# Performance work log

Hardware: AMD Instinct MI355X
Metric: run time of the kernel (lower is better)

## Reference

```python
import jax, jax.numpy as jnp
import numpy as np

KERNEL = 9
EPS = 1e-5


def build_time_adj(t, kernel=KERNEL):
    # Faithful port of time_edge_index + utils.add_self_loops (all weights 1).
    # At[target, source] = 1 ; PyG edge list rows were [source=i, target=neighbor].
    p = (kernel - 1) // 2
    edges = []
    for i in range(t):
        if i < p:
            num_zeros_before = p - i
            elems = kernel - 1 - num_zeros_before
            before = i
            after = elems - before
            for j in range(before, 0, -1):
                edges.append((i, i - j))
            for j in range(after, 0, -1):
                edges.append((i, i + j))
        elif t - i <= p:
            num_zeros_after = p - (t - i) + 1
            elems = kernel - 1 - num_zeros_after
            before = kernel - 1 - p
            after = elems - before
            for j in range(before, 0, -1):
                edges.append((i, i - j))
            for j in range(after, 0, -1):
                edges.append((i, i + j))
        else:
            for j in range(1, p + 1):
                edges.append((i, i - j))
                edges.append((i, i + j))
    At = np.zeros((t, t), dtype=np.float32)
    for s, tg in edges:
        At[tg, s] = 1.0
    At[np.arange(t), np.arange(t)] = 1.0  # add_self_loops
    return At


def setup_inputs() -> dict:
    key = jax.random.key(0)
    ks = jax.random.split(key, 8)
    B, T, V, C = 64, 300, 25, 64
    x = jax.random.normal(ks[0], (B, T, V, C), dtype=jnp.float32)
    A = jax.random.uniform(ks[1], (3, V, V), dtype=jnp.float32)
    edge_importance = jnp.ones((3, V, V), dtype=jnp.float32)
    scale = 0.125  # ~xavier for 64x64
    W1 = jax.random.normal(ks[2], (C, C), dtype=jnp.float32) * scale
    W2 = jax.random.normal(ks[3], (C, C), dtype=jnp.float32) * scale
    W3 = jax.random.normal(ks[4], (C, C), dtype=jnp.float32) * scale
    Wt = jax.random.normal(ks[5], (C, C), dtype=jnp.float32) * scale
    b1 = jnp.zeros((C,), jnp.float32)
    b2 = jnp.zeros((C,), jnp.float32)
    b3 = jnp.zeros((C,), jnp.float32)
    bt = jnp.zeros((C,), jnp.float32)
    gamma = jnp.ones((C,), jnp.float32)
    beta = jnp.zeros((C,), jnp.float32)
    return {"x": x, "A": A, "edge_importance": edge_importance,
            "W1": W1, "b1": b1, "W2": W2, "b2": b2, "W3": W3, "b3": b3,
            "Wt": Wt, "bt": bt, "gamma": gamma, "beta": beta}


def reference(x, A, edge_importance, W1, b1, W2, b2, W3, b3, Wt, bt, gamma, beta):
    B, T, V, C = x.shape
    I = jnp.eye(V, dtype=x.dtype)
    Ae = A * edge_importance  # [3,V,V]

    # ---- Net_nodes: 3 spatial GCNConv branches summed (gcn_norm, self-loops) ----
    out = jnp.zeros((B, T, V, W1.shape[1]), dtype=x.dtype)
    for Ai, W, b in ((Ae[0], W1, b1), (Ae[1], W2, b2), (Ae[2], W3, b3)):
        Ad = Ai * (1.0 - I) + I                      # fill_diag(adj, 1.0)
        d = Ad.sum(axis=1)
        dinv = jnp.where(d > 0, d ** -0.5, 0.0)
        An = dinv[:, None] * Ad * dinv[None, :]      # D^-1/2 (A+I) D^-1/2
        out = out + jnp.einsum('vu,btuc->btvc', An, x @ W) + b

    def bn(h):  # BatchNorm2d over (B,T,V) per channel, training-mode stats
        m = h.mean(axis=(0, 1, 2))
        v = h.var(axis=(0, 1, 2))
        return (h - m) * jax.lax.rsqrt(v + EPS) * gamma + beta

    h = jax.nn.relu(bn(out))

    # ---- temporal GCNConv (normalize=False, unit edge weights, self loops) ----
    At = jnp.asarray(build_time_adj(T))              # [T,T] banded 0/1
    h = jnp.einsum('ts,bsvc->btvc', At, h @ Wt) + bt

    h = bn(h)  # same bn_2d module reused; dropout is identity in eval
    # residual=False, stride=1 -> x_res = 0, no sampling
    return jax.nn.relu(h)
```

## Files before the change

### kernel.cpp

```cpp
#include <hip/hip_runtime.h>

typedef unsigned short u16;
typedef unsigned int   u32;
typedef _Float16       f16;
typedef _Float16 f16x8 __attribute__((ext_vector_type(8)));
typedef float    f32x4 __attribute__((ext_vector_type(4)));

#define B_  64
#define T_  300
#define V_  25
#define C_  64
#define ROWS (B_*T_)
#define ROWE (V_*C_)
#define NSTAT 480000.0f
#define EPS_ 1e-5f
#define TTILE 30
#define K2GRID 4800

__device__ __forceinline__ float b2f(u16 u) {
    union { u32 i; float f; } v; v.i = ((u32)u) << 16; return v.f;
}
__device__ __forceinline__ u16 f2b(float f) {
    union { float f; u32 i; } v; v.f = f;
    u32 x = v.i;
    u32 r = x + 0x7fffu + ((x >> 16) & 1u);
    return (u16)(r >> 16);
}
__device__ __forceinline__ u32 pk2h(float a, float b) {
    union { f16 h[2]; u32 u; } p;
    p.h[0] = (f16)a; p.h[1] = (f16)b;
    return p.u;
}
__device__ __forceinline__ u16 h2u(float v) {
    union { f16 h; u16 u; } p; p.h = (f16)v; return p.u;
}
__device__ __forceinline__ float u2h(u16 u) {
    union { u16 u; f16 h; } p; p.u = u; return (float)p.h;
}

template<bool F32>
__device__ __forceinline__ float ldv(const void* p, size_t i) {
    if (F32) return ((const float*)p)[i];
    return b2f(((const u16*)p)[i]);
}

template<bool F32> struct Geo { static const int STR = F32 ? 3200 : 1600; };

__global__ void k0_detect(const void* W1raw, int* flag)
{
    __shared__ float red[256];
    const u16* p = (const u16*)W1raw;
    float mx = 0.0f;
    for (int i = threadIdx.x; i < 4096; i += 256) {
        float v = fabsf(b2f(p[i]));
        if (v == v) mx = fmaxf(mx, v);
    }
    red[threadIdx.x] = mx;
    __syncthreads();
    for (int s = 128; s > 0; s >>= 1) {
        if (threadIdx.x < s) red[threadIdx.x] = fmaxf(red[threadIdx.x], red[threadIdx.x + s]);
        __syncthreads();
    }
    if (threadIdx.x == 0) flag[0] = (red[0] > 1e10f) ? 1 : 0;
}

template<bool F32>
__global__ void k1_prep(const int* __restrict__ flag,
                        const void* A, const void* E,
                        const void* W1, const void* W2, const void* W3,
                        const void* Wt,
                        const void* b1, const void* b2, const void* b3,
                        u16* __restrict__ anf, u16* __restrict__ wcatT,
                        u16* __restrict__ wtT, float* __restrict__ bsum)
{
    if (flag[0] != (F32 ? 1 : 0)) return;
    __shared__ float dinvL[75];
    const int tid = threadIdx.x;
    if (tid < 75) {
        int i = tid / 25, v = tid % 25;
        float d = 1.0f;
        for (int u = 0; u < 25; ++u)
            if (u != v) d += ldv<F32>(A, (i*25+v)*25+u) * ldv<F32>(E, (i*25+v)*25+u);
        dinvL[tid] = (d > 0.0f) ? rsqrtf(d) : 0.0f;
    }
    __syncthreads();
    for (int idx = tid; idx < 3072; idx += 256) {
        int fr = idx >> 9, lane = (idx >> 3) & 63, j = idx & 7;
        int i = fr >> 1, nt = fr & 1;
        int v = nt*16 + (lane & 15);
        int u = ((lane >> 4) << 3) + j;
        float val = 0.0f;
        if (v < 25 && u < 25) {
            float ad = (u == v) ? 1.0f
                     : ldv<F32>(A, (i*25+v)*25+u) * ldv<F32>(E, (i*25+v)*25+u);
            val = dinvL[i*25+v] * ad * dinvL[i*25+u];
        }
        anf[idx] = h2u(val);
    }
    for (int idx = tid; idx < 13824; idx += 256) {
        int i = idx / 4608;
        int rem = idx - i*4608;
        int c = rem / 72, k = rem - (rem/72)*72;
        float val = 0.0f;
        if (k < 64) {
            const void* W = (i == 0) ? W1 : ((i == 1) ? W2 : W3);
            val = ldv<F32>(W, k*64 + c);
        }
        wcatT[idx] = h2u(val);
    }
    for (int idx = tid; idx < 4608; idx += 256) {
        int c = idx / 72, k = idx - (idx/72)*72;
        float val = (k < 64) ? ldv<F32>(Wt, k*64 + c) : 0.0f;
        wtT[idx] = h2u(val);
    }
    if (tid < 64) bsum[tid] = ldv<F32>(b1, tid) + ldv<F32>(b2, tid) + ldv<F32>(b3, tid);
}

template<bool F32>
__global__ __launch_bounds__(256, 3) void k2_mfma(
    const int* __restrict__ flag, const void* x,
    const u16* __restrict__ wcatT, const u16* __restrict__ anf,
    const float* __restrict__ bsum,
    u16* __restrict__ out1, float* __restrict__ p1)
{
    if (flag[0] != (F32 ? 1 : 0)) return;
    const int STR = Geo<F32>::STR;

    __shared__ f16 xf[112*72];
    __shared__ u16 xw[256*40];

    const int tid  = threadIdx.x;
    const int lane = tid & 63, w = tid >> 6;
    const int r0   = blockIdx.x * 4;

    for (int q4 = tid; q4 < 1600; q4 += 256) {
        int r = (q4 * 10486) >> 22;
        int rem = q4 - 400*r;
        float v0, v1, v2, v3;
        if (F32) {
            float4 t4 = ((const float4*)x)[(size_t)(r0+r)*400 + rem];
            v0 = t4.x; v1 = t4.y; v2 = t4.z; v3 = t4.w;
        } else {
            ushort4 t4 = ((const ushort4*)x)[(size_t)(r0+r)*400 + rem];
            v0 = b2f(t4.x); v1 = b2f(t4.y); v2 = b2f(t4.z); v3 = b2f(t4.w);
        }
        int u = rem >> 4, k0 = (rem & 15) << 2;
        int m = r*28 + u;
        *(uint2*)&xf[m*72 + k0] = make_uint2(pk2h(v0, v1), pk2h(v2, v3));
    }
    for (int idx = tid; idx < 432; idx += 256) {
        int j  = (idx * 57) >> 11;
        int off = idx - 36*j;
        int rr = (j*11) >> 5, p = j - 3*rr;
        ((u32*)xf)[(rr*28 + 25 + p)*36 + off] = 0u;
    }
    *(uint2*)&xw[tid*40 + 28] = make_uint2(0u, 0u);

    f16x8 anfr[3][2];
    #pragma unroll
    for (int i = 0; i < 3; ++i)
        #pragma unroll
        for (int nt = 0; nt < 2; ++nt)
            anfr[i][nt] = *(const f16x8*)&anf[((i*2 + nt)*64 + lane)*8];

    const int c0 = w*16 + ((lane >> 4) << 2);
    float bs[4];
    #pragma unroll
    for (int t = 0; t < 4; ++t) bs[t] = bsum[c0 + t];

    f32x4 acc[4][2];
    #pragma unroll
    for (int j = 0; j < 4; ++j) {
        acc[j][0] = f32x4{0.f, 0.f, 0.f, 0.f};
        acc[j][1] = f32x4{0.f, 0.f, 0.f, 0.f};
    }

    __syncthreads();

    #pragma unroll
    for (int i = 0; i < 3; ++i) {
        f16x8 wfr[4][2];
        #pragma unroll
        for (int nt = 0; nt < 4; ++nt)
            #pragma unroll
            for (int ks = 0; ks < 2; ++ks)
                wfr[nt][ks] = *(const f16x8*)&wcatT[
                    (i*64 + nt*16 + (lane & 15))*72 + ks*32 + ((lane >> 4) << 3)];

        for (int mt = w; mt < 7; mt += 4) {
            const int arow = (mt*16 + (lane & 15))*72 + ((lane >> 4) << 3);
            f16x8 a0 = *(const f16x8*)&xf[arow];
            f16x8 a1 = *(const f16x8*)&xf[arow + 32];
            const int m0 = mt*16 + ((lane >> 4) << 2);
            const int r  = (m0 * 293) >> 13;
            const int u0 = m0 - 28*r;
            #pragma unroll
            for (int nt = 0; nt < 4; ++nt) {
                f32x4 d = f32x4{0.f, 0.f, 0.f, 0.f};
                d = __builtin_amdgcn_mfma_f32_16x16x32_f16(a0, wfr[nt][0], d, 0, 0, 0);
                d = __builtin_amdgcn_mfma_f32_16x16x32_f16(a1, wfr[nt][1], d, 0, 0, 0);
                const int cc = nt*16 + (lane & 15);
                *(uint2*)&xw[(r*64 + cc)*40 + u0] =
                    make_uint2(pk2h(d[0], d[1]), pk2h(d[2], d[3]));
            }
        }
        __syncthreads();

        #pragma unroll
        for (int j = 0; j < 4; ++j) {
            const int mt2 = w + 4*j;
            f16x8 a = *(const f16x8*)&xw[(mt2*16 + (lane & 15))*40 + ((lane >> 4) << 3)];
            acc[j][0] = __builtin_amdgcn_mfma_f32_16x16x32_f16(a, anfr[i][0], acc[j][0], 0, 0, 0);
            acc[j][1] = __builtin_amdgcn_mfma_f32_16x16x32_f16(a, anfr[i][1], acc[j][1], 0, 0, 0);
        }
        __syncthreads();
    }

    float ssum[4] = {0.f, 0.f, 0.f, 0.f}, ssq[4] = {0.f, 0.f, 0.f, 0.f};
    const int vb = lane & 15;
    #pragma unroll
    for (int j = 0; j < 4; ++j) {
        #pragma unroll
        for (int nt = 0; nt < 2; ++nt) {
            const int v = nt*16 + vb;
            if (v < 25) {
                float o0 = acc[j][nt][0] + bs[0];
                float o1 = acc[j][nt][1] + bs[1];
                float o2 = acc[j][nt][2] + bs[2];
                float o3 = acc[j][nt][3] + bs[3];
                ssum[0] += o0; ssq[0] += o0*o0;
                ssum[1] += o1; ssq[1] += o1*o1;
                ssum[2] += o2; ssq[2] += o2*o2;
                ssum[3] += o3; ssq[3] += o3*o3;
                ushort4 pk;
                pk.x = f2b(o0); pk.y = f2b(o1); pk.z = f2b(o2); pk.w = f2b(o3);
                *(ushort4*)&out1[(size_t)(r0 + j)*STR + v*64 + c0] = pk;
            }
        }
    }
    #pragma unroll
    for (int t = 0; t < 4; ++t) {
        #pragma unroll
        for (int off = 1; off < 16; off <<= 1) {
            ssum[t] += __shfl_xor(ssum[t], off);
            ssq[t]  += __shfl_xor(ssq[t],  off);
        }
    }
    if ((lane & 15) == 0) {
        #pragma unroll
        for (int t = 0; t < 4; ++t) {
            p1[(size_t)blockIdx.x*128 + c0 + t]      = ssum[t];
            p1[(size_t)blockIdx.x*128 + 64 + c0 + t] = ssq[t];
        }
    }
}

template<bool F32>
__global__ void k_bnstats(const int* __restrict__ flag,
                          const float* __restrict__ part, int nblk,
                          const void* gamma, const void* beta,
                          float* __restrict__ scale, float* __restrict__ shift)
{
    if (flag[0] != (F32 ? 1 : 0)) return;
    __shared__ float redL[2048];
    const int tid = threadIdx.x, c = tid & 63, q = tid >> 6;
    float s = 0.0f, ss = 0.0f;
    for (int p = q; p < nblk; p += 16) { s += part[p*128 + c]; ss += part[p*128 + 64 + c]; }
    redL[q*64 + c] = s; redL[1024 + q*64 + c] = ss;
    __syncthreads();
    for (int h = 8; h > 0; h >>= 1) {
        if (q < h) {
            redL[q*64 + c]        += redL[(q+h)*64 + c];
            redL[1024 + q*64 + c] += redL[1024 + (q+h)*64 + c];
        }
        __syncthreads();
    }
    if (tid < 64) {
        const float S  = redL[tid];
        const float SS = redL[1024 + tid];
        const float m   = S / NSTAT;
        const float var = SS / NSTAT - m*m;
        const float rstd = rsqrtf(var + EPS_);
        const float sc = ldv<F32>(gamma, tid) * rstd;
        scale[tid] = sc;
        shift[tid] = ldv<F32>(beta, tid) - m * sc;
    }
}

template<bool F32>
__global__ __launch_bounds__(128) void k_halo(const int* __restrict__ flag,
                                              const u16* out1, u16* halo)
{
    if (flag[0] != (F32 ? 1 : 0)) return;
    const int STR = Geo<F32>::STR;
    const int id = blockIdx.x;
    const int slot = id & 7, tile = (id >> 3) % 10, b = id / 80;
    const int t = tile * TTILE + (slot < 4 ? slot : slot + 22);
    const uint4* src = (const uint4*)&out1[((size_t)b*T_ + t) * STR];
    uint4* dst = (uint4*)&halo[(size_t)id * ROWE];
    for (int j = threadIdx.x; j < 200; j += 128) dst[j] = src[j];
}

template<bool F32>
__device__ __forceinline__ const u16* row_ptr(const u16* out1, const u16* halo,
                                              int b, int s, int t0)
{
    if (s >= t0 && s < t0 + TTILE)
        return &out1[((size_t)b*T_ + s) * Geo<F32>::STR];
    const int tile = s / TTILE, rem = s % TTILE;
    const int slot = rem < 4 ? rem : rem - 22;
    return &halo[(((size_t)b*10 + tile)*8 + slot) * ROWE];
}

template<bool F32>
__global__ __launch_bounds__(256, 3) void k3_temporal(
    const int* __restrict__ flag,
    u16* out1, const u16* __restrict__ halo,
    const u16* __restrict__ wtT, const void* bt,
    const float* __restrict__ sc1, const float* __restrict__ sh1,
    float* __restrict__ p2)
{
    if (flag[0] != (F32 ? 1 : 0)) return;
    const int STR = Geo<F32>::STR;

    __shared__ u16   ring[10*1600];
    __shared__ f16   hsumH[32*72];
    __shared__ u16   zL[1600];
    __shared__ float redL[256];

    const int tid = threadIdx.x, lane = tid & 63, w = tid >> 6;
    const int b = blockIdx.y, t0 = blockIdx.x * TTILE;
    const bool act = (tid < 200);

    for (int i = tid; i < 252; i += 256) ((u32*)&hsumH[25*72])[i] = 0u;

    float hacc[8];
    #pragma unroll
    for (int e = 0; e < 8; ++e) hacc[e] = 0.0f;
    const int c0u = (tid*8) & 63;
    const int vrow = tid >> 3;
    float S1[8], H1[8];
    #pragma unroll
    for (int e = 0; e < 8; ++e) { S1[e] = sc1[c0u+e]; H1[e] = sh1[c0u+e]; }

    const int ntp = w >> 1, mt = w & 1;
    f16x8 wfr[2][2];
    #pragma unroll
    for (int ntl = 0; ntl < 2; ++ntl)
        #pragma unroll
        for (int ks = 0; ks < 2; ++ks)
            wfr[ntl][ks] = *(const f16x8*)&wtT[
                ((ntp*2+ntl)*16 + (lane & 15))*72 + ks*32 + ((lane >> 4) << 3)];
    float btv[2];
    #pragma unroll
    for (int ntl = 0; ntl < 2; ++ntl)
        btv[ntl] = ldv<F32>(bt, (ntp*2+ntl)*16 + (lane & 15));

    {
        int slo = t0 - 4; if (slo < 0) slo = 0;
        for (int s = slo; s <= t0 + 4; ++s) {
            const u16* xr = row_ptr<F32>(out1, halo, b, s, t0);
            if (act) {
                uint4 xv = *(const uint4*)&xr[tid*8];
                const u16* xs = (const u16*)&xv;
                u16 hb[8];
                #pragma unroll
                for (int e = 0; e < 8; ++e) {
                    float hv = fmaf(b2f(xs[e]), S1[e], H1[e]);
                    hv = hv > 0.0f ? hv : 0.0f;
                    hb[e] = f2b(hv);
                    hacc[e] += b2f(hb[e]);
                }
                *(uint4*)&ring[(s%10)*1600 + tid*8] = *(uint4*)hb;
            }
        }
        if (act) {
            u16 hs[8];
            #pragma unroll
            for (int e = 0; e < 8; ++e) hs[e] = h2u(hacc[e]);
            *(uint4*)&hsumH[vrow*72 + c0u] = *(uint4*)hs;
        }
    }
    __syncthreads();

    float zs[2] = {0.f, 0.f}, zq[2] = {0.f, 0.f};

    for (int t = t0; t < t0 + TTILE; ++t) {
        {
            const int arow = (mt*16 + (lane & 15))*72 + ((lane >> 4) << 3);
            f16x8 a0 = *(const f16x8*)&hsumH[arow];
            f16x8 a1 = *(const f16x8*)&hsumH[arow + 32];
            #pragma unroll
            for (int ntl = 0; ntl < 2; ++ntl) {
                f32x4 d = f32x4{btv[ntl], btv[ntl], btv[ntl], btv[ntl]};
                d = __builtin_amdgcn_mfma_f32_16x16x32_f16(a0, wfr[ntl][0], d, 0, 0, 0);
                d = __builtin_amdgcn_mfma_f32_16x16x32_f16(a1, wfr[ntl][1], d, 0, 0, 0);
                const int cc = (ntp*2+ntl)*16 + (lane & 15);
                #pragma unroll
                for (int j = 0; j < 4; ++j) {
                    const int v = mt*16 + ((lane >> 4) << 2) + j;
                    if (v < 25) {
                        zs[ntl] += d[j]; zq[ntl] += d[j]*d[j];
                        zL[v*64 + cc] = h2u(d[j]);
                    }
                }
            }
        }
        __syncthreads();

        if (tid < 200)
            *(uint4*)&out1[((size_t)b*T_ + t)*STR + tid*8] = ((const uint4*)zL)[tid];

        if (t + 1 < t0 + TTILE) {
            const int snew = t + 5, sold = t - 4;
            if (act) {
                if (snew < T_) {
                    const u16* xr = row_ptr<F32>(out1, halo, b, snew, t0);
                    uint4 xv = *(const uint4*)&xr[tid*8];
                    const u16* xs = (const u16*)&xv;
                    u16 hb[8];
                    #pragma unroll
                    for (int e = 0; e < 8; ++e) {
                        float hv = fmaf(b2f(xs[e]), S1[e], H1[e]);
                        hv = hv > 0.0f ? hv : 0.0f;
                        hb[e] = f2b(hv);
                        hacc[e] += b2f(hb[e]);
                    }
                    *(uint4*)&ring[(snew%10)*1600 + tid*8] = *(uint4*)hb;
                }
                if (sold >= 0) {
                    uint4 ov = *(const uint4*)&ring[(sold%10)*1600 + tid*8];
                    const u16* os = (const u16*)&ov;
                    #pragma unroll
                    for (int e = 0; e < 8; ++e) hacc[e] -= b2f(os[e]);
                }
                u16 hs[8];
                #pragma unroll
                for (int e = 0; e < 8; ++e) hs[e] = h2u(hacc[e]);
                *(uint4*)&hsumH[vrow*72 + c0u] = *(uint4*)hs;
            }
        }
        __syncthreads();
    }

    #pragma unroll
    for (int ntl = 0; ntl < 2; ++ntl) {
        #pragma unroll
        for (int off = 16; off < 64; off <<= 1) {
            zs[ntl] += __shfl_xor(zs[ntl], off);
            zq[ntl] += __shfl_xor(zq[ntl], off);
        }
    }
    if (lane < 16) {
        redL[w*32 + lane]        = zs[0];
        redL[w*32 + 16 + lane]   = zs[1];
        redL[128 + w*32 + lane]      = zq[0];
        redL[128 + w*32 + 16 + lane] = zq[1];
    }
    __syncthreads();
    if (tid < 64) {
        const int c = tid;
        const int ntg = c >> 4, pr = ntg >> 1, ntl = ntg & 1, l = c & 15;
        const int w0 = pr*2, w1 = pr*2 + 1;
        float s = redL[w0*32 + ntl*16 + l] + redL[w1*32 + ntl*16 + l];
        float q = redL[128 + w0*32 + ntl*16 + l] + redL[128 + w1*32 + ntl*16 + l];
        const int blk = blockIdx.y * (T_/TTILE) + blockIdx.x;
        p2[(size_t)blk*128 + c]      = s;
        p2[(size_t)blk*128 + 64 + c] = q;
    }
}

template<bool F32>
__global__ __launch_bounds__(256) void k4_final(
    const int* __restrict__ flag,
    const float* __restrict__ sc2, const float* __restrict__ sh2,
    void* outp)
{
    if (flag[0] != (F32 ? 1 : 0)) return;
    const int STR = Geo<F32>::STR;
    const int tid = threadIdx.x;
    const int c0u = (tid*8) & 63;
    float S2[8], H2[8];
    #pragma unroll
    for (int e = 0; e < 8; ++e) { S2[e] = sc2[c0u+e]; H2[e] = sh2[c0u+e]; }
    const int r0 = blockIdx.x * 10;
    u16* z = (u16*)outp;

    for (int r = 0; r < 10; ++r) {
        const int row = r0 + r;
        uint4 zv;
        if (tid < 200) zv = *(const uint4*)&z[(size_t)row*STR + tid*8];
        __syncthreads();
        if (tid < 200) {
            const u16* zp = (const u16*)&zv;
            float o[8];
            #pragma unroll
            for (int e = 0; e < 8; ++e) {
                float oo = fmaf(u2h(zp[e]), S2[e], H2[e]);
                o[e] = oo > 0.0f ? oo : 0.0f;
            }
            if (F32) {
                float* dst = (float*)outp + (size_t)row*ROWE + tid*8;
                *(float4*)dst     = float4{o[0], o[1], o[2], o[3]};
                *(float4*)(dst+4) = float4{o[4], o[5], o[6], o[7]};
            } else {
                u16 ob[8];
                #pragma unroll
                for (int e = 0; e < 8; ++e) ob[e] = f2b(o[e]);
                *(uint4*)&((u16*)outp)[(size_t)row*ROWE + tid*8] = *(uint4*)ob;
            }
        }
    }
}

extern "C" void kernel_launch(void* const* d_in, const int* in_sizes, int n_in,
                              void* d_out, int out_size, void* d_ws, size_t ws_size,
                              hipStream_t stream)
{
    const void* x     = d_in[0];
    const void* A     = d_in[1];
    const void* E     = d_in[2];
    const void* W1    = d_in[3];
    const void* b1    = d_in[4];
    const void* W2    = d_in[5];
    const void* b2    = d_in[6];
    const void* W3    = d_in[7];
    const void* b3    = d_in[8];
    const void* Wt    = d_in[9];
    const void* bt    = d_in[10];
    const void* gamma = d_in[11];
    const void* beta  = d_in[12];

    u16* out1 = (u16*)d_out;

    int*   flag = (int*)d_ws;
    float* wsf  = (float*)d_ws;
    float* bsum = wsf + 4;
    float* sc1  = bsum + 64;
    float* sh1  = sc1 + 64;
    float* sc2  = sh1 + 64;
    float* sh2  = sc2 + 64;
    float* p1   = sh2 + 64;
    float* p2   = p1 + (size_t)K2GRID*128;
    u16*  halo  = (u16*)(p2 + 640*128);
    u16*  wcatT = halo + (size_t)5120*1600;
    u16*  anf   = wcatT + 13824;
    u16*  wtT   = anf + 3072;

    hipLaunchKernelGGL(k0_detect, dim3(1), dim3(256), 0, stream, W1, flag);

    hipLaunchKernelGGL(k1_prep<false>, dim3(1), dim3(256), 0, stream,
                       flag, A, E, W1, W2, W3, Wt, b1, b2, b3, anf, wcatT, wtT, bsum);
    hipLaunchKernelGGL(k1_prep<true>, dim3(1), dim3(256), 0, stream,
                       flag, A, E, W1, W2, W3, Wt, b1, b2, b3, anf, wcatT, wtT, bsum);

    hipLaunchKernelGGL(k2_mfma<false>, dim3(K2GRID), dim3(256), 0, stream,
                       flag, x, wcatT, anf, bsum, out1, p1);
    hipLaunchKernelGGL(k2_mfma<true>, dim3(K2GRID), dim3(256), 0, stream,
                       flag, x, wcatT, anf, bsum, out1, p1);

    hipLaunchKernelGGL(k_bnstats<false>, dim3(1), dim3(1024), 0, stream,
                       flag, p1, K2GRID, gamma, beta, sc1, sh1);
    hipLaunchKernelGGL(k_bnstats<true>, dim3(1), dim3(1024), 0, stream,
                       flag, p1, K2GRID, gamma, beta, sc1, sh1);

    hipLaunchKernelGGL(k_halo<false>, dim3(5120), dim3(128), 0, stream,
                       flag, out1, halo);
    hipLaunchKernelGGL(k_halo<true>, dim3(5120), dim3(128), 0, stream,
                       flag, out1, halo);

    hipLaunchKernelGGL(k3_temporal<false>, dim3(10, 64), dim3(256), 0, stream,
                       flag, out1, halo, wtT, bt, sc1, sh1, p2);
    hipLaunchKernelGGL(k3_temporal<true>, dim3(10, 64), dim3(256), 0, stream,
                       flag, out1, halo, wtT, bt, sc1, sh1, p2);

    hipLaunchKernelGGL(k_bnstats<false>, dim3(1), dim3(1024), 0, stream,
                       flag, p2, 640, gamma, beta, sc2, sh2);
    hipLaunchKernelGGL(k_bnstats<true>, dim3(1), dim3(1024), 0, stream,
                       flag, p2, 640, gamma, beta, sc2, sh2);

    hipLaunchKernelGGL(k4_final<false>, dim3(1920), dim3(256), 0, stream,
                       flag, sc2, sh2, d_out);
    hipLaunchKernelGGL(k4_final<true>, dim3(1920), dim3(256), 0, stream,
                       flag, sc2, sh2, d_out);
}
```

Measured before the change: 491.9 us.

## Restructure spatial GCN kernel per-wave, fuse halo copy, split BN stat reduction

```diff
diff --git a/kernel.cpp b/kernel.cpp
--- a/kernel.cpp
+++ b/kernel.cpp
@@ -15,7 +15,8 @@
 #define NSTAT 480000.0f
 #define EPS_ 1e-5f
 #define TTILE 30
-#define K2GRID 4800
+#define K2BLK 1200
+#define NWID  4800
 
 __device__ __forceinline__ float b2f(u16 u) {
     union { u32 i; float f; } v; v.i = ((u32)u) << 16; return v.f;
@@ -120,185 +121,180 @@
 __global__ __launch_bounds__(256, 3) void k2_mfma(
     const int* __restrict__ flag, const void* x,
     const u16* __restrict__ wcatT, const u16* __restrict__ anf,
-    const float* __restrict__ bsum,
-    u16* __restrict__ out1, float* __restrict__ p1)
+    u16* __restrict__ out1, u16* __restrict__ halo, float* __restrict__ p1)
 {
     if (flag[0] != (F32 ? 1 : 0)) return;
     const int STR = Geo<F32>::STR;
 
-    __shared__ f16 xf[112*72];
-    __shared__ u16 xw[256*40];
-
-    const int tid  = threadIdx.x;
-    const int lane = tid & 63, w = tid >> 6;
-    const int r0   = blockIdx.x * 4;
-
-    for (int q4 = tid; q4 < 1600; q4 += 256) {
-        int r = (q4 * 10486) >> 22;
-        int rem = q4 - 400*r;
-        float v0, v1, v2, v3;
-        if (F32) {
-            float4 t4 = ((const float4*)x)[(size_t)(r0+r)*400 + rem];
-            v0 = t4.x; v1 = t4.y; v2 = t4.z; v3 = t4.w;
-        } else {
-            ushort4 t4 = ((const ushort4*)x)[(size_t)(r0+r)*400 + rem];
-            v0 = b2f(t4.x); v1 = b2f(t4.y); v2 = b2f(t4.z); v3 = b2f(t4.w);
-        }
-        int u = rem >> 4, k0 = (rem & 15) << 2;
-        int m = r*28 + u;
-        *(uint2*)&xf[m*72 + k0] = make_uint2(pk2h(v0, v1), pk2h(v2, v3));
-    }
-    for (int idx = tid; idx < 432; idx += 256) {
-        int j  = (idx * 57) >> 11;
-        int off = idx - 36*j;
-        int rr = (j*11) >> 5, p = j - 3*rr;
-        ((u32*)xf)[(rr*28 + 25 + p)*36 + off] = 0u;
-    }
-    *(uint2*)&xw[tid*40 + 28] = make_uint2(0u, 0u);
-
-    f16x8 anfr[3][2];
+    __shared__ f16 xfS[4][32*64];
+    __shared__ u16 xwS[4][64*64];
+
+    const int tid = threadIdx.x, lane = tid & 63, w = tid >> 6;
+    const int lo = lane & 15, hi = lane >> 4;
+    f16* xf = xfS[w];
+    u16* xw = xwS[w];
+
+    for (int q = lane; q < 224; q += 64) ((u32*)xf)[800 + q] = 0u;
+
+    const int wid = blockIdx.x*4 + w;
+
+    float ss[16], sq[16];
     #pragma unroll
-    for (int i = 0; i < 3; ++i)
-        #pragma unroll
-        for (int nt = 0; nt < 2; ++nt)
-            anfr[i][nt] = *(const f16x8*)&anf[((i*2 + nt)*64 + lane)*8];
-
-    const int c0 = w*16 + ((lane >> 4) << 2);
-    float bs[4];
+    for (int i = 0; i < 16; ++i) { ss[i] = 0.0f; sq[i] = 0.0f; }
+
+    #pragma unroll 1
+    for (int rr = 0; rr < 4; ++rr) {
+        const int row = wid*4 + rr;
+
+        for (int q = lane; q < 200; q += 64) {
+            const int u = q >> 3, g = q & 7;
+            float v0,v1,v2,v3,v4,v5,v6,v7;
+            if (F32) {
+                float4 a4 = ((const float4*)x)[(size_t)row*400 + q*2];
+                float4 b4 = ((const float4*)x)[(size_t)row*400 + q*2 + 1];
+                v0=a4.x; v1=a4.y; v2=a4.z; v3=a4.w;
+                v4=b4.x; v5=b4.y; v6=b4.z; v7=b4.w;
+            } else {
+                union { uint4 u4; u16 s[8]; } t4;
+                t4.u4 = ((const uint4*)x)[(size_t)row*200 + q];
+                v0=b2f(t4.s[0]); v1=b2f(t4.s[1]); v2=b2f(t4.s[2]); v3=b2f(t4.s[3]);
+                v4=b2f(t4.s[4]); v5=b2f(t4.s[5]); v6=b2f(t4.s[6]); v7=b2f(t4.s[7]);
+            }
+            uint4 st = make_uint4(pk2h(v0,v1), pk2h(v2,v3), pk2h(v4,v5), pk2h(v6,v7));
+            *(uint4*)&xf[u*64 + ((g ^ (u & 7)) << 3)] = st;
+        }
+
+        f32x4 acc[4][2];
+        #pragma unroll
+        for (int m = 0; m < 4; ++m) {
+            acc[m][0] = f32x4{0.f,0.f,0.f,0.f};
+            acc[m][1] = f32x4{0.f,0.f,0.f,0.f};
+        }
+
+        #pragma unroll 1
+        for (int i = 0; i < 3; ++i) {
+            f16x8 wfr[4][2];
+            #pragma unroll
+            for (int nt = 0; nt < 4; ++nt)
+                #pragma unroll
+                for (int ks = 0; ks < 2; ++ks)
+                    wfr[nt][ks] = *(const f16x8*)&wcatT[
+                        (size_t)(i*64 + nt*16 + lo)*72 + ks*32 + (hi << 3)];
+            f16x8 an0 = *(const f16x8*)&anf[((i*2 + 0)*64 + lane)*8];
+            f16x8 an1 = *(const f16x8*)&anf[((i*2 + 1)*64 + lane)*8];
+
+            #pragma unroll
+            for (int mt = 0; mt < 2; ++mt) {
+                const int mrow = mt*16 + lo;
+                f16x8 a0 = *(const f16x8*)&xf[mrow*64 + ((hi ^ (lo & 7)) << 3)];
+                f16x8 a1 = *(const f16x8*)&xf[mrow*64 + (((4|hi) ^ (lo & 7)) << 3)];
+                const int gu  = mt*2 + (hi >> 1);
+                const int off = (hi & 1)*4;
+                #pragma unroll
+                for (int nt = 0; nt < 4; ++nt) {
+                    f32x4 d = f32x4{0.f,0.f,0.f,0.f};
+                    d = __builtin_amdgcn_mfma_f32_16x16x32_f16(a0, wfr[nt][0], d, 0, 0, 0);
+                    d = __builtin_amdgcn_mfma_f32_16x16x32_f16(a1, wfr[nt][1], d, 0, 0, 0);
+                    const int c = nt*16 + lo;
+                    *(uint2*)&xw[c*64 + ((gu ^ (lo & 7)) << 3) + off] =
+                        make_uint2(pk2h(d[0], d[1]), pk2h(d[2], d[3]));
+                }
+            }
+
+            #pragma unroll
+            for (int mt2 = 0; mt2 < 4; ++mt2) {
+                f16x8 a = *(const f16x8*)&xw[(mt2*16 + lo)*64 + ((hi ^ (lo & 7)) << 3)];
+                acc[mt2][0] = __builtin_amdgcn_mfma_f32_16x16x32_f16(a, an0, acc[mt2][0], 0, 0, 0);
+                acc[mt2][1] = __builtin_amdgcn_mfma_f32_16x16x32_f16(a, an1, acc[mt2][1], 0, 0, 0);
+            }
+        }
+
+        const int b = row / T_;
+        const int t = row - b*T_;
+        const int tm = t % TTILE;
+        const bool hbd = (tm < 4) || (tm >= TTILE - 4);
+        u16* hrow = nullptr;
+        if (hbd) {
+            const int slot = tm < 4 ? tm : tm - 22;
+            hrow = halo + (((size_t)b*10 + t/TTILE)*8 + slot)*ROWE;
+        }
+        u16* orow = out1 + (size_t)row*STR;
+        #pragma unroll
+        for (int mt2 = 0; mt2 < 4; ++mt2) {
+            const int c0 = mt2*16 + hi*4;
+            #pragma unroll
+            for (int nt2 = 0; nt2 < 2; ++nt2) {
+                const int v = nt2*16 + lo;
+                const float o0 = acc[mt2][nt2][0];
+                const float o1 = acc[mt2][nt2][1];
+                const float o2 = acc[mt2][nt2][2];
+                const float o3 = acc[mt2][nt2][3];
+                ss[mt2*4+0] += o0; sq[mt2*4+0] += o0*o0;
+                ss[mt2*4+1] += o1; sq[mt2*4+1] += o1*o1;
+                ss[mt2*4+2] += o2; sq[mt2*4+2] += o2*o2;
+                ss[mt2*4+3] += o3; sq[mt2*4+3] += o3*o3;
+                if (v < 25) {
+                    ushort4 pk;
+                    pk.x = f2b(o0); pk.y = f2b(o1); pk.z = f2b(o2); pk.w = f2b(o3);
+                    *(ushort4*)&orow[v*64 + c0] = pk;
+                    if (hbd) *(ushort4*)&hrow[v*64 + c0] = pk;
+                }
+            }
+        }
+    }
+
     #pragma unroll
-    for (int t = 0; t < 4; ++t) bs[t] = bsum[c0 + t];
-
-    f32x4 acc[4][2];
-    #pragma unroll
-    for (int j = 0; j < 4; ++j) {
-        acc[j][0] = f32x4{0.f, 0.f, 0.f, 0.f};
-        acc[j][1] = f32x4{0.f, 0.f, 0.f, 0.f};
-    }
-
-    __syncthreads();
-
-    #pragma unroll
-    for (int i = 0; i < 3; ++i) {
-        f16x8 wfr[4][2];
-        #pragma unroll
-        for (int nt = 0; nt < 4; ++nt)
-            #pragma unroll
-            for (int ks = 0; ks < 2; ++ks)
-                wfr[nt][ks] = *(const f16x8*)&wcatT[
-                    (i*64 + nt*16 + (lane & 15))*72 + ks*32 + ((lane >> 4) << 3)];
-
-        for (int mt = w; mt < 7; mt += 4) {
-            const int arow = (mt*16 + (lane & 15))*72 + ((lane >> 4) << 3);
-            f16x8 a0 = *(const f16x8*)&xf[arow];
-            f16x8 a1 = *(const f16x8*)&xf[arow + 32];
-            const int m0 = mt*16 + ((lane >> 4) << 2);
-            const int r  = (m0 * 293) >> 13;
-            const int u0 = m0 - 28*r;
-            #pragma unroll
-            for (int nt = 0; nt < 4; ++nt) {
-                f32x4 d = f32x4{0.f, 0.f, 0.f, 0.f};
-                d = __builtin_amdgcn_mfma_f32_16x16x32_f16(a0, wfr[nt][0], d, 0, 0, 0);
-                d = __builtin_amdgcn_mfma_f32_16x16x32_f16(a1, wfr[nt][1], d, 0, 0, 0);
-                const int cc = nt*16 + (lane & 15);
-                *(uint2*)&xw[(r*64 + cc)*40 + u0] =
-                    make_uint2(pk2h(d[0], d[1]), pk2h(d[2], d[3]));
-            }
-        }
-        __syncthreads();
-
-        #pragma unroll
-        for (int j = 0; j < 4; ++j) {
-            const int mt2 = w + 4*j;
-            f16x8 a = *(const f16x8*)&xw[(mt2*16 + (lane & 15))*40 + ((lane >> 4) << 3)];
-            acc[j][0] = __builtin_amdgcn_mfma_f32_16x16x32_f16(a, anfr[i][0], acc[j][0], 0, 0, 0);
-            acc[j][1] = __builtin_amdgcn_mfma_f32_16x16x32_f16(a, anfr[i][1], acc[j][1], 0, 0, 0);
-        }
-        __syncthreads();
-    }
-
-    float ssum[4] = {0.f, 0.f, 0.f, 0.f}, ssq[4] = {0.f, 0.f, 0.f, 0.f};
-    const int vb = lane & 15;
-    #pragma unroll
-    for (int j = 0; j < 4; ++j) {
-        #pragma unroll
-        for (int nt = 0; nt < 2; ++nt) {
-            const int v = nt*16 + vb;
-            if (v < 25) {
-                float o0 = acc[j][nt][0] + bs[0];
-                float o1 = acc[j][nt][1] + bs[1];
-                float o2 = acc[j][nt][2] + bs[2];
-                float o3 = acc[j][nt][3] + bs[3];
-                ssum[0] += o0; ssq[0] += o0*o0;
-                ssum[1] += o1; ssq[1] += o1*o1;
-                ssum[2] += o2; ssq[2] += o2*o2;
-                ssum[3] += o3; ssq[3] += o3*o3;
-                ushort4 pk;
-                pk.x = f2b(o0); pk.y = f2b(o1); pk.z = f2b(o2); pk.w = f2b(o3);
-                *(ushort4*)&out1[(size_t)(r0 + j)*STR + v*64 + c0] = pk;
-            }
-        }
-    }
-    #pragma unroll
-    for (int t = 0; t < 4; ++t) {
+    for (int si = 0; si < 16; ++si) {
         #pragma unroll
         for (int off = 1; off < 16; off <<= 1) {
-            ssum[t] += __shfl_xor(ssum[t], off);
-            ssq[t]  += __shfl_xor(ssq[t],  off);
-        }
-    }
-    if ((lane & 15) == 0) {
-        #pragma unroll
-        for (int t = 0; t < 4; ++t) {
-            p1[(size_t)blockIdx.x*128 + c0 + t]      = ssum[t];
-            p1[(size_t)blockIdx.x*128 + 64 + c0 + t] = ssq[t];
-        }
-    }
+            ss[si] += __shfl_xor(ss[si], off);
+            sq[si] += __shfl_xor(sq[si], off);
+        }
+    }
+    if (lo == 0) {
+        #pragma unroll
+        for (int si = 0; si < 16; ++si) {
+            const int c = (si >> 2)*16 + hi*4 + (si & 3);
+            p1[(size_t)wid*128 + c]      = ss[si];
+            p1[(size_t)wid*128 + 64 + c] = sq[si];
+        }
+    }
+}
+
+__global__ __launch_bounds__(128) void k_reduce(const float* __restrict__ in,
+                                                int n, float* __restrict__ outq)
+{
+    const int t = threadIdx.x;
+    float s = 0.0f;
+    for (int r = blockIdx.x; r < n; r += 64) s += in[(size_t)r*128 + t];
+    outq[(size_t)blockIdx.x*128 + t] = s;
 }
 
 template<bool F32>
 __global__ void k_bnstats(const int* __restrict__ flag,
-                          const float* __restrict__ part, int nblk,
+                          const float* __restrict__ q,
                           const void* gamma, const void* beta,
+                          const float* __restrict__ mb, int useb,
                           float* __restrict__ scale, float* __restrict__ shift)
 {
     if (flag[0] != (F32 ? 1 : 0)) return;
-    __shared__ float redL[2048];
-    const int tid = threadIdx.x, c = tid & 63, q = tid >> 6;
-    float s = 0.0f, ss = 0.0f;
-    for (int p = q; p < nblk; p += 16) { s += part[p*128 + c]; ss += part[p*128 + 64 + c]; }
-    redL[q*64 + c] = s; redL[1024 + q*64 + c] = ss;
+    __shared__ float redL[512];
+    const int tid = threadIdx.x, c = tid & 63, g = tid >> 6;
+    float s = 0.0f, ssq = 0.0f;
+    for (int r = g; r < 64; r += 4) { s += q[r*128 + c]; ssq += q[r*128 + 64 + c]; }
+    redL[g*64 + c] = s; redL[256 + g*64 + c] = ssq;
     __syncthreads();
-    for (int h = 8; h > 0; h >>= 1) {
-        if (q < h) {
-            redL[q*64 + c]        += redL[(q+h)*64 + c];
-            redL[1024 + q*64 + c] += redL[1024 + (q+h)*64 + c];
-        }
-        __syncthreads();
-    }
     if (tid < 64) {
-        const float S  = redL[tid];
-        const float SS = redL[1024 + tid];
-        const float m   = S / NSTAT;
-        const float var = SS / NSTAT - m*m;
+        const float S  = redL[tid] + redL[64+tid] + redL[128+tid] + redL[192+tid];
+        const float SS = redL[256+tid] + redL[320+tid] + redL[384+tid] + redL[448+tid];
+        const float my  = S / NSTAT;
+        const float var = SS / NSTAT - my*my;
+        const float m   = my + (useb ? mb[tid] : 0.0f);
         const float rstd = rsqrtf(var + EPS_);
         const float sc = ldv<F32>(gamma, tid) * rstd;
         scale[tid] = sc;
         shift[tid] = ldv<F32>(beta, tid) - m * sc;
     }
-}
-
-template<bool F32>
-__global__ __launch_bounds__(128) void k_halo(const int* __restrict__ flag,
-                                              const u16* out1, u16* halo)
-{
-    if (flag[0] != (F32 ? 1 : 0)) return;
-    const int STR = Geo<F32>::STR;
-    const int id = blockIdx.x;
-    const int slot = id & 7, tile = (id >> 3) % 10, b = id / 80;
-    const int t = tile * TTILE + (slot < 4 ? slot : slot + 22);
-    const uint4* src = (const uint4*)&out1[((size_t)b*T_ + t) * STR];
-    uint4* dst = (uint4*)&halo[(size_t)id * ROWE];
-    for (int j = threadIdx.x; j < 200; j += 128) dst[j] = src[j];
 }
 
 template<bool F32>
@@ -452,8 +448,8 @@
         }
     }
     if (lane < 16) {
-        redL[w*32 + lane]        = zs[0];
-        redL[w*32 + 16 + lane]   = zs[1];
+        redL[w*32 + lane]            = zs[0];
+        redL[w*32 + 16 + lane]       = zs[1];
         redL[128 + w*32 + lane]      = zq[0];
         redL[128 + w*32 + 16 + lane] = zq[1];
     }
@@ -477,38 +473,54 @@
     void* outp)
 {
     if (flag[0] != (F32 ? 1 : 0)) return;
-    const int STR = Geo<F32>::STR;
     const int tid = threadIdx.x;
-    const int c0u = (tid*8) & 63;
-    float S2[8], H2[8];
-    #pragma unroll
-    for (int e = 0; e < 8; ++e) { S2[e] = sc2[c0u+e]; H2[e] = sh2[c0u+e]; }
-    const int r0 = blockIdx.x * 10;
-    u16* z = (u16*)outp;
-
-    for (int r = 0; r < 10; ++r) {
-        const int row = r0 + r;
-        uint4 zv;
-        if (tid < 200) zv = *(const uint4*)&z[(size_t)row*STR + tid*8];
-        __syncthreads();
-        if (tid < 200) {
-            const u16* zp = (const u16*)&zv;
-            float o[8];
+
+    if (!F32) {
+        const size_t NQ = (size_t)ROWS * 200;
+        const size_t stride = (size_t)gridDim.x * blockDim.x;
+        size_t q = (size_t)blockIdx.x * blockDim.x + tid;
+        const int c0 = ((int)(q & 7)) * 8;
+        float S2[8], H2[8];
+        #pragma unroll
+        for (int e = 0; e < 8; ++e) { S2[e] = sc2[c0+e]; H2[e] = sh2[c0+e]; }
+        u16* z = (u16*)outp;
+        for (; q < NQ; q += stride) {
+            union { uint4 u4; u16 s[8]; } zv;
+            zv.u4 = *(const uint4*)&z[q*8];
+            u16 ob[8];
             #pragma unroll
             for (int e = 0; e < 8; ++e) {
-                float oo = fmaf(u2h(zp[e]), S2[e], H2[e]);
-                o[e] = oo > 0.0f ? oo : 0.0f;
-            }
-            if (F32) {
+                float oo = fmaf(u2h(zv.s[e]), S2[e], H2[e]);
+                ob[e] = f2b(oo > 0.0f ? oo : 0.0f);
+            }
+            *(uint4*)&z[q*8] = *(uint4*)ob;
+        }
+    } else {
+        const int STR = Geo<true>::STR;
+        const int c0u = (tid*8) & 63;
+        float S2[8], H2[8];
+        #pragma unroll
+        for (int e = 0; e < 8; ++e) { S2[e] = sc2[c0u+e]; H2[e] = sh2[c0u+e]; }
+        const int r0 = blockIdx.x * 10;
+        u16* z = (u16*)outp;
+        for (int r = 0; r < 10; ++r) {
+            const int row = r0 + r;
+            uint4 zv;
+            if (tid < 200) zv = *(const uint4*)&z[(size_t)row*STR + tid*8];
+            __syncthreads();
+            if (tid < 200) {
+                const u16* zp = (const u16*)&zv;
+                float o[8];
+                #pragma unroll
+                for (int e = 0; e < 8; ++e) {
+                    float oo = fmaf(u2h(zp[e]), S2[e], H2[e]);
+                    o[e] = oo > 0.0f ? oo : 0.0f;
+                }
                 float* dst = (float*)outp + (size_t)row*ROWE + tid*8;
                 *(float4*)dst     = float4{o[0], o[1], o[2], o[3]};
                 *(float4*)(dst+4) = float4{o[4], o[5], o[6], o[7]};
-            } else {
-                u16 ob[8];
-                #pragma unroll
-                for (int e = 0; e < 8; ++e) ob[e] = f2b(o[e]);
-                *(uint4*)&((u16*)outp)[(size_t)row*ROWE + tid*8] = *(uint4*)ob;
-            }
+            }
+            __syncthreads();
         }
     }
 }
@@ -541,46 +553,55 @@
     float* sc2  = sh1 + 64;
     float* sh2  = sc2 + 64;
     float* p1   = sh2 + 64;
-    float* p2   = p1 + (size_t)K2GRID*128;
-    u16*  halo  = (u16*)(p2 + 640*128);
+    float* p2   = p1 + (size_t)NWID*128;
+    float* q1   = p2 + 640*128;
+    float* q2   = q1 + 64*128;
+    u16*  halo  = (u16*)(q2 + 64*128);
     u16*  wcatT = halo + (size_t)5120*1600;
     u16*  anf   = wcatT + 13824;
     u16*  wtT   = anf + 3072;
 
+    const long NX = (long)B_*T_*V_*C_;
+    int mode = -1;
+    if (n_in > 0) {
+        if      (in_sizes[0] == (int)(NX*2)) mode = 0;
+        else if (in_sizes[0] == (int)(NX*4)) mode = 1;
+    }
+    const bool do_b = (mode != 1), do_f = (mode != 0);
+
     hipLaunchKernelGGL(k0_detect, dim3(1), dim3(256), 0, stream, W1, flag);
 
-    hipLaunchKernelGGL(k1_prep<false>, dim3(1), dim3(256), 0, stream,
+    if (do_b) hipLaunchKernelGGL(k1_prep<false>, dim3(1), dim3(256), 0, stream,
                        flag, A, E, W1, W2, W3, Wt, b1, b2, b3, anf, wcatT, wtT, bsum);
-    hipLaunchKernelGGL(k1_prep<true>, dim3(1), dim3(256), 0, stream,
+    if (do_f) hipLaunchKernelGGL(k1_prep<true>, dim3(1), dim3(256), 0, stream,
                        flag, A, E, W1, W2, W3, Wt, b1, b2, b3, anf, wcatT, wtT, bsum);
 
-    hipLaunchKernelGGL(k2_mfma<false>, dim3(K2GRID), dim3(256), 0, stream,
-                       flag, x, wcatT, anf, bsum, out1, p1);
-    hipLaunchKernelGGL(k2_mfma<true>, dim3(K2GRID), dim3(256), 0, stream,
-                       flag, x, wcatT, anf, bsum, out1, p1);
-
-    hipLaunchKernelGGL(k_bnstats<false>, dim3(1), dim3(1024), 0, stream,
-                       flag, p1, K2GRID, gamma, beta, sc1, sh1);
-    hipLaunchKernelGGL(k_bnstats<true>, dim3(1), dim3(1024), 0, stream,
-                       flag, p1, K2GRID, gamma, beta, sc1, sh1);
-
-    hipLaunchKernelGGL(k_halo<false>, dim3(5120), dim3(128), 0, stream,
-                       flag, out1, halo);
-    hipLaunchKernelGGL(k_halo<true>, dim3(5120), dim3(128), 0, stream,
-                       flag, out1, halo);
-
-    hipLaunchKernelGGL(k3_temporal<false>, dim3(10, 64), dim3(256), 0, stream,
+    if (do_b) hipLaunchKernelGGL(k2_mfma<false>, dim3(K2BLK), dim3(256), 0, stream,
+                       flag, x, wcatT, anf, out1, halo, p1);
+    if (do_f) hipLaunchKernelGGL(k2_mfma<true>, dim3(K2BLK), dim3(256), 0, stream,
+                       flag, x, wcatT, anf, out1, halo, p1);
+
+    hipLaunchKernelGGL(k_reduce, dim3(64), dim3(128), 0, stream, p1, NWID, q1);
+
+    if (do_b) hipLaunchKernelGGL(k_bnstats<false>, dim3(1), dim3(256), 0, stream,
+                       flag, q1, gamma, beta, bsum, 1, sc1, sh1);
+    if (do_f) hipLaunchKernelGGL(k_bnstats<true>, dim3(1), dim3(256), 0, stream,
+                       flag, q1, gamma, beta, bsum, 1, sc1, sh1);
+
+    if (do_b) hipLaunchKernelGGL(k3_temporal<false>, dim3(10, 64), dim3(256), 0, stream,
                        flag, out1, halo, wtT, bt, sc1, sh1, p2);
-    hipLaunchKernelGGL(k3_temporal<true>, dim3(10, 64), dim3(256), 0, stream,
+    if (do_f) hipLaunchKernelGGL(k3_temporal<true>, dim3(10, 64), dim3(256), 0, stream,
                        flag, out1, halo, wtT, bt, sc1, sh1, p2);
 
-    hipLaunchKernelGGL(k_bnstats<false>, dim3(1), dim3(1024), 0, stream,
-                       flag, p2, 640, gamma, beta, sc2, sh2);
-    hipLaunchKernelGGL(k_bnstats<true>, dim3(1), dim3(1024), 0, stream,
-                       flag, p2, 640, gamma, beta, sc2, sh2);
-
-    hipLaunchKernelGGL(k4_final<false>, dim3(1920), dim3(256), 0, stream,
+    hipLaunchKernelGGL(k_reduce, dim3(64), dim3(128), 0, stream, p2, 640, q2);
+
+    if (do_b) hipLaunchKernelGGL(k_bnstats<false>, dim3(1), dim3(256), 0, stream,
+                       flag, q2, gamma, beta, bsum, 0, sc2, sh2);
+    if (do_f) hipLaunchKernelGGL(k_bnstats<true>, dim3(1), dim3(256), 0, stream,
+                       flag, q2, gamma, beta, bsum, 0, sc2, sh2);
+
+    if (do_b) hipLaunchKernelGGL(k4_final<false>, dim3(2048), dim3(256), 0, stream,
                        flag, sc2, sh2, d_out);
-    hipLaunchKernelGGL(k4_final<true>, dim3(1920), dim3(256), 0, stream,
+    if (do_f) hipLaunchKernelGGL(k4_final<true>, dim3(1920), dim3(256), 0, stream,
                        flag, sc2, sh2, d_out);
 }
```

Result: faster. 439.8 us (-10.6%).
